# Performance work log

Measured on AMD Instinct MI355X. Metric: run time of the kernel, lower is better.

## Reference

```python
import jax, jax.numpy as jnp
import numpy as np
from jax import lax

B, N, DDESC = 8, 256, 128
COST_KP = 1.0
COST_DESC = 1.0
BLOCK = 128  # row block for L1 cdist


def setup_inputs() -> dict:
    key = jax.random.key(0)
    k1, k2, k3, k4, k5 = jax.random.split(key, 5)
    W, H = 640, 480
    wh = jnp.array([W, H], jnp.float32)
    kp1 = jax.random.uniform(k1, (B, N, 2)) * wh          # pixel coords
    kp2 = jax.random.uniform(k2, (B, N, 2)) * wh
    desc1 = jax.random.normal(k3, (B, N, DDESC))
    desc2 = jax.random.normal(k4, (B, N, DDESC))
    theta = jax.random.uniform(k5, (1,)) * (2.0 * jnp.pi)
    return {
        "theta": theta,
        "my_feature": jnp.concatenate([kp1, desc1], -1),
        "my_tf_feature": jnp.concatenate([kp2, desc2], -1),
        "my_width": W,
        "my_height": H,
    }


def _fundamental_8point(p1, p2):
    """Normalized 8-point algorithm (cv2.FM_8POINT): p2^T F p1 = 0, F[2,2]=1."""
    def norm(p):
        m = p.mean(0)
        d = jnp.sqrt(((p - m) ** 2).sum(1)).mean()
        s = jnp.sqrt(2.0) / d
        T = jnp.array([[1.0, 0.0, 0.0], [0.0, 1.0, 0.0], [0.0, 0.0, 0.0]]) * s \
            + jnp.zeros((3, 3)).at[0, 2].set(-s * m[0]).at[1, 2].set(-s * m[1]).at[2, 2].set(1.0)
        return (p - m) * s, T
    x1, T1 = norm(p1)
    x2, T2 = norm(p2)
    u1, v1 = x1[:, 0], x1[:, 1]
    u2, v2 = x2[:, 0], x2[:, 1]
    A = jnp.stack([u2 * u1, u2 * v1, u2, v2 * u1, v2 * v1, v2, u1, v1, jnp.ones_like(u1)], 1)
    _, _, Vt = jnp.linalg.svd(A, full_matrices=False)      # Vt: [9,9]
    Fm = Vt[-1].reshape(3, 3)
    U, S, Vt2 = jnp.linalg.svd(Fm)
    Fm = (U * S.at[2].set(0.0)) @ Vt2                      # enforce rank 2
    Fm = T2.T @ Fm @ T1
    return Fm / Fm[2, 2]


def _cdist_l1(a, b):
    """torch.cdist(p=1) without materializing [M,M,D]; blocked over rows."""
    M, D = a.shape
    ab = a.reshape(M // BLOCK, BLOCK, D)
    rows = lax.map(lambda blk: jnp.abs(blk[:, None, :] - b[None, :, :]).sum(-1), ab)
    return rows.reshape(M, b.shape[0])


def _cost_matrix(theta, my_feature, my_tf_feature, W, H):
    my_kp = my_feature[..., :2]
    my_tf_kp = my_tf_feature[..., :2]
    my_desc = my_feature[..., 2:]
    my_tf_desc = my_tf_feature[..., 2:]

    c, s = jnp.cos(theta[0]), jnp.sin(theta[0])
    zero = jnp.zeros(())
    one = jnp.ones(())
    Tm = jnp.stack([
        jnp.stack([c, -s, zero, zero]),
        jnp.stack([s, c, zero, zero]),
        jnp.stack([zero, zero, one, zero]),
        jnp.stack([zero, zero, zero, one]),
    ])  # make_transformation_M(theta, 0, 0): z-rotation, no translation

    # homogeneous image-centered coords: [B, 4, N]
    all_kp = jnp.stack([
        my_kp[:, :, 0] - 0.5 * W,
        -my_kp[:, :, 1] + 0.5 * H,
        jnp.zeros_like(my_kp[:, :, 0]),
        jnp.ones_like(my_kp[:, :, 0]),
    ], 1)
    cal = jnp.round(jnp.einsum('ij,bjn->bin', Tm, all_kp))[:, :2, :]  # [B,2,N]
    g = cal.transpose(0, 2, 1)                                        # [B,N,2]
    o = jnp.stack([g[..., 0] + 0.5 * W, -g[..., 1] + 0.5 * H], -1)    # back to pixels

    pts1 = my_tf_kp.astype(jnp.int32).reshape(B * N, 2).astype(jnp.float32)
    pts2 = o.astype(jnp.int32).reshape(B * N, 2).astype(jnp.float32)
    F = _fundamental_8point(pts1, pts2)

    ones = jnp.ones((B * N, 1), jnp.float32)
    p1h = jnp.concatenate([pts1, ones], 1)
    p2h = jnp.concatenate([pts2, ones], 1)
    cost_kp = jnp.abs((p1h @ F.astype(jnp.float32)) @ p2h.T)          # [BN, BN]

    cost_desc = _cdist_l1(my_desc.reshape(B * N, -1), my_tf_desc.reshape(B * N, -1))
    C = COST_KP * cost_kp + COST_DESC * cost_desc
    return C.reshape(B, N, B * N)


def _hungarian_np(cost):
    """scipy.optimize.linear_sum_assignment (JV shortest augmenting path), numpy."""
    cost = np.asarray(cost, dtype=np.float64)
    n = cost.shape[0]
    u = np.zeros(n)
    v = np.zeros(n)
    path = np.full(n, -1, dtype=np.int64)
    col4row = np.full(n, -1, dtype=np.int64)
    row4col = np.full(n, -1, dtype=np.int64)
    for cur_row in range(n):
        shortest = np.full(n, np.inf)
        remaining = np.ones(n, dtype=bool)
        SR = []
        i = cur_row
        min_val = 0.0
        sink = -1
        while sink == -1:
            SR.append(i)
            idx = np.nonzero(remaining)[0]
            r = min_val + cost[i, idx] - u[i] - v[idx]
            better = r < shortest[idx]
            bidx = idx[better]
            shortest[bidx] = r[better]
            path[bidx] = i
            jpos = idx[np.argmin(shortest[idx])]
            min_val = shortest[jpos]
            remaining[jpos] = False
            if row4col[jpos] == -1:
                sink = jpos
            else:
                i = row4col[jpos]
        u[cur_row] += min_val
        for i2 in SR:
            if i2 != cur_row:
                u[i2] += min_val - shortest[col4row[i2]]
        scanned = ~remaining
        v[scanned] -= min_val - shortest[scanned]
        j = sink
        while True:
            i2 = path[j]
            row4col[j] = i2
            col4row[i2], j = j, col4row[i2]
            if i2 == cur_row:
                break
    return col4row


def reference(theta, my_feature, my_tf_feature, my_width, my_height):
    C = _cost_matrix(theta, my_feature, my_tf_feature, float(my_width), float(my_height))
    Cn = np.asarray(jax.device_get(C))
    # diagonal [N,N] blocks: C.split(num_kp, -1) -> c[i] in the torch code
    cols = np.stack([_hungarian_np(Cn[i, :, i * N:(i + 1) * N]) for i in range(B)])
    rows = np.tile(np.arange(N), (B, 1))
    matches = jnp.asarray(np.stack([rows, cols], 1), dtype=jnp.int32)  # [B,2,N]
    return C, matches
```

## Files before the change

kernel.cpp:

```cpp
#include <hip/hip_runtime.h>
#include <hip/hip_bf16.h>
#include <cfloat>
#include <math.h>

#define BB 8
#define NN 256
#define BN 2048
#define DD 128
#define FEAT 130

__global__ __launch_bounds__(256) void prep_kernel(
    const float* __restrict__ theta,
    const float* __restrict__ feat1,
    const float* __restrict__ feat2,
    const int* __restrict__ wp, const int* __restrict__ hp,
    float* __restrict__ pts1, float* __restrict__ pts2) {
  int i = blockIdx.x * 256 + threadIdx.x;
  if (i >= BN) return;
  double W = (double)wp[0], H = (double)hp[0];
  double th = (double)theta[0];
  double c = cos(th), s = sin(th);
  double kx = (double)feat1[(size_t)i * FEAT + 0];
  double ky = (double)feat1[(size_t)i * FEAT + 1];
  double x = kx - 0.5 * W;
  double y = -ky + 0.5 * H;
  double calx = rint(c * x - s * y);
  double caly = rint(s * x + c * y);
  double ox = calx + 0.5 * W;
  double oy = -caly + 0.5 * H;
  pts2[2 * i]     = (float)(int)ox;
  pts2[2 * i + 1] = (float)(int)oy;
  pts1[2 * i]     = (float)(int)feat2[(size_t)i * FEAT + 0];
  pts1[2 * i + 1] = (float)(int)feat2[(size_t)i * FEAT + 1];
}

__device__ inline double wred(double x) {
#pragma unroll
  for (int off = 32; off > 0; off >>= 1) x += __shfl_down(x, off, 64);
  return x;
}

#define JROT(P, Q) {                                                          \
  double app_ = __shfl(Bc[P], P);                                             \
  double aqq_ = __shfl(Bc[Q], Q);                                             \
  double apq_ = __shfl(Bc[P], Q);                                             \
  double c_, s_;                                                              \
  if (fabs(apq_) > 1e-300) {                                                  \
    double tau_ = (aqq_ - app_) / (2.0 * apq_);                               \
    double t_ = (tau_ >= 0.0 ? 1.0 : -1.0) / (fabs(tau_) + sqrt(1.0 + tau_ * tau_)); \
    c_ = 1.0 / sqrt(1.0 + t_ * t_);                                           \
    s_ = t_ * c_;                                                             \
  } else { c_ = 1.0; s_ = 0.0; }                                              \
  const int prt_ = (jln == P) ? Q : ((jln == Q) ? P : jln);                   \
  const bool isP_ = (jln == P), isQ_ = (jln == Q);                            \
  _Pragma("unroll")                                                           \
  for (int ii = 0; ii < 9; ++ii) {                                            \
    double ob_ = __shfl(Bc[ii], prt_);                                        \
    double ov_ = __shfl(Vc[ii], prt_);                                        \
    if (isP_) { Bc[ii] = c_ * Bc[ii] - s_ * ob_; Vc[ii] = c_ * Vc[ii] - s_ * ov_; } \
    if (isQ_) { Bc[ii] = s_ * ob_ + c_ * Bc[ii]; Vc[ii] = s_ * ov_ + c_ * Vc[ii]; } \
  }                                                                           \
  { double rp_ = Bc[P], rq_ = Bc[Q];                                          \
    Bc[P] = c_ * rp_ - s_ * rq_; Bc[Q] = s_ * rp_ + c_ * rq_; } }

#define ROT3(P, Q) {                                                          \
  double apq_ = A3[P][Q];                                                     \
  double c_, s_;                                                              \
  if (fabs(apq_) > 1e-300) {                                                  \
    double tau_ = (A3[Q][Q] - A3[P][P]) / (2.0 * apq_);                       \
    double t_ = (tau_ >= 0.0 ? 1.0 : -1.0) / (fabs(tau_) + sqrt(1.0 + tau_ * tau_)); \
    c_ = 1.0 / sqrt(1.0 + t_ * t_); s_ = t_ * c_;                             \
  } else { c_ = 1.0; s_ = 0.0; }                                              \
  _Pragma("unroll")                                                           \
  for (int ii = 0; ii < 3; ++ii) { double a_ = A3[ii][P], b_ = A3[ii][Q];     \
    A3[ii][P] = c_ * a_ - s_ * b_; A3[ii][Q] = s_ * a_ + c_ * b_; }           \
  _Pragma("unroll")                                                           \
  for (int ii = 0; ii < 3; ++ii) { double a_ = A3[P][ii], b_ = A3[Q][ii];     \
    A3[P][ii] = c_ * a_ - s_ * b_; A3[Q][ii] = s_ * a_ + c_ * b_; }           \
  _Pragma("unroll")                                                           \
  for (int ii = 0; ii < 3; ++ii) { double a_ = V3[ii][P], b_ = V3[ii][Q];     \
    V3[ii][P] = c_ * a_ - s_ * b_; V3[ii][Q] = s_ * a_ + c_ * b_; } }

__global__ __launch_bounds__(256) void fmat_kernel(
    const float* __restrict__ pts1f, const float* __restrict__ pts2f,
    double* __restrict__ Fout) {
  __shared__ double sred[6];
  __shared__ double sATA[45];
  __shared__ double sV[9][16];
  __shared__ double sEv[16];
  const int tid = threadIdx.x;
  const int lane = tid & 63;
  if (tid < 6) sred[tid] = 0.0;
  if (tid < 45) sATA[tid] = 0.0;
  __syncthreads();

  double sx1 = 0, sy1 = 0, sx2 = 0, sy2 = 0;
  for (int p = tid; p < BN; p += 256) {
    sx1 += (double)pts1f[2 * p];     sy1 += (double)pts1f[2 * p + 1];
    sx2 += (double)pts2f[2 * p];     sy2 += (double)pts2f[2 * p + 1];
  }
  sx1 = wred(sx1); sy1 = wred(sy1); sx2 = wred(sx2); sy2 = wred(sy2);
  if (lane == 0) {
    atomicAdd(&sred[0], sx1); atomicAdd(&sred[1], sy1);
    atomicAdd(&sred[2], sx2); atomicAdd(&sred[3], sy2);
  }
  __syncthreads();
  const double m1x = sred[0] * (1.0 / BN), m1y = sred[1] * (1.0 / BN);
  const double m2x = sred[2] * (1.0 / BN), m2y = sred[3] * (1.0 / BN);

  double d1 = 0, d2 = 0;
  for (int p = tid; p < BN; p += 256) {
    double ax = (double)pts1f[2 * p] - m1x, ay = (double)pts1f[2 * p + 1] - m1y;
    double bx = (double)pts2f[2 * p] - m2x, by = (double)pts2f[2 * p + 1] - m2y;
    d1 += sqrt(ax * ax + ay * ay);
    d2 += sqrt(bx * bx + by * by);
  }
  d1 = wred(d1); d2 = wred(d2);
  if (lane == 0) { atomicAdd(&sred[4], d1); atomicAdd(&sred[5], d2); }
  __syncthreads();
  const double s1 = sqrt(2.0) / (sred[4] * (1.0 / BN));
  const double s2 = sqrt(2.0) / (sred[5] * (1.0 / BN));

  double acc45[45];
#pragma unroll
  for (int e = 0; e < 45; ++e) acc45[e] = 0.0;
  for (int p = tid; p < BN; p += 256) {
    double u1 = ((double)pts1f[2 * p]     - m1x) * s1;
    double v1 = ((double)pts1f[2 * p + 1] - m1y) * s1;
    double u2 = ((double)pts2f[2 * p]     - m2x) * s2;
    double v2 = ((double)pts2f[2 * p + 1] - m2y) * s2;
    double r[9] = {u2 * u1, u2 * v1, u2, v2 * u1, v2 * v1, v2, u1, v1, 1.0};
#pragma unroll
    for (int a = 0; a < 9; ++a)
#pragma unroll
      for (int b = a; b < 9; ++b)
        acc45[9 * a - (a * (a - 1)) / 2 + (b - a)] += r[a] * r[b];
  }
#pragma unroll
  for (int e = 0; e < 45; ++e) {
    double vv = wred(acc45[e]);
    if (lane == 0) atomicAdd(&sATA[e], vv);
  }
  __syncthreads();

  if (tid < 64) {
    const int jln = tid;
    double Bc[9], Vc[9];
#pragma unroll
    for (int i2 = 0; i2 < 9; ++i2) {
      if (jln < 9) {
        int a = i2 < jln ? i2 : jln;
        int b = i2 < jln ? jln : i2;
        Bc[i2] = sATA[9 * a - (a * (a - 1)) / 2 + (b - a)];
      } else Bc[i2] = 0.0;
      Vc[i2] = (i2 == jln) ? 1.0 : 0.0;
    }
    for (int sw = 0; sw < 7; ++sw) {
      JROT(0,1) JROT(0,2) JROT(0,3) JROT(0,4) JROT(0,5) JROT(0,6) JROT(0,7) JROT(0,8)
      JROT(1,2) JROT(1,3) JROT(1,4) JROT(1,5) JROT(1,6) JROT(1,7) JROT(1,8)
      JROT(2,3) JROT(2,4) JROT(2,5) JROT(2,6) JROT(2,7) JROT(2,8)
      JROT(3,4) JROT(3,5) JROT(3,6) JROT(3,7) JROT(3,8)
      JROT(4,5) JROT(4,6) JROT(4,7) JROT(4,8)
      JROT(5,6) JROT(5,7) JROT(5,8)
      JROT(6,7) JROT(6,8)
      JROT(7,8)
    }
    double ev = 0.0;
#pragma unroll
    for (int i2 = 0; i2 < 9; ++i2) if (jln == i2) ev = Bc[i2];
    if (jln < 9) {
      sEv[jln] = ev;
#pragma unroll
      for (int i2 = 0; i2 < 9; ++i2) sV[i2][jln] = Vc[i2];
    }
  }
  __syncthreads();

  if (tid == 0) {
    int jm = 0; double be = sEv[0];
#pragma unroll
    for (int jj = 1; jj < 9; ++jj) if (sEv[jj] < be) { be = sEv[jj]; jm = jj; }
    double F0[9];
#pragma unroll
    for (int i2 = 0; i2 < 9; ++i2) F0[i2] = sV[i2][jm];
    double M00 = F0[0], M01 = F0[1], M02 = F0[2];
    double M10 = F0[3], M11 = F0[4], M12 = F0[5];
    double M20 = F0[6], M21 = F0[7], M22 = F0[8];
    double A3[3][3], V3[3][3];
    A3[0][0] = M00*M00 + M10*M10 + M20*M20;
    A3[0][1] = M00*M01 + M10*M11 + M20*M21;
    A3[0][2] = M00*M02 + M10*M12 + M20*M22;
    A3[1][1] = M01*M01 + M11*M11 + M21*M21;
    A3[1][2] = M01*M02 + M11*M12 + M21*M22;
    A3[2][2] = M02*M02 + M12*M12 + M22*M22;
    A3[1][0] = A3[0][1]; A3[2][0] = A3[0][2]; A3[2][1] = A3[1][2];
#pragma unroll
    for (int ii = 0; ii < 3; ++ii)
#pragma unroll
      for (int jj = 0; jj < 3; ++jj) V3[ii][jj] = (ii == jj) ? 1.0 : 0.0;
    for (int sw = 0; sw < 10; ++sw) { ROT3(0,1) ROT3(0,2) ROT3(1,2) }
    double w0 = A3[0][0], w1 = A3[1][1], w2 = A3[2][2];
    double vx, vy, vz;
    if (w0 <= w1 && w0 <= w2)      { vx = V3[0][0]; vy = V3[1][0]; vz = V3[2][0]; }
    else if (w1 <= w2)             { vx = V3[0][1]; vy = V3[1][1]; vz = V3[2][1]; }
    else                           { vx = V3[0][2]; vy = V3[1][2]; vz = V3[2][2]; }
    double Mv0 = M00 * vx + M01 * vy + M02 * vz;
    double Mv1 = M10 * vx + M11 * vy + M12 * vz;
    double Mv2 = M20 * vx + M21 * vy + M22 * vz;
    double F200 = M00 - Mv0 * vx, F201 = M01 - Mv0 * vy, F202 = M02 - Mv0 * vz;
    double F210 = M10 - Mv1 * vx, F211 = M11 - Mv1 * vy, F212 = M12 - Mv1 * vz;
    double F220 = M20 - Mv2 * vx, F221 = M21 - Mv2 * vy, F222 = M22 - Mv2 * vz;
    double R00 = s2 * F200, R01 = s2 * F201, R02 = s2 * F202;
    double R10 = s2 * F210, R11 = s2 * F211, R12 = s2 * F212;
    double R20 = -s2 * m2x * F200 - s2 * m2y * F210 + F220;
    double R21 = -s2 * m2x * F201 - s2 * m2y * F211 + F221;
    double R22 = -s2 * m2x * F202 - s2 * m2y * F212 + F222;
    double D00 = s1 * R00, D10 = s1 * R10, D20 = s1 * R20;
    double D01 = s1 * R01, D11 = s1 * R11, D21 = s1 * R21;
    double D02 = -s1 * m1x * R00 - s1 * m1y * R01 + R02;
    double D12 = -s1 * m1x * R10 - s1 * m1y * R11 + R12;
    double D22 = -s1 * m1x * R20 - s1 * m1y * R21 + R22;
    Fout[0] = D00 / D22; Fout[1] = D01 / D22; Fout[2] = D02 / D22;
    Fout[3] = D10 / D22; Fout[4] = D11 / D22; Fout[5] = D12 / D22;
    Fout[6] = D20 / D22; Fout[7] = D21 / D22; Fout[8] = D22 / D22;
  }
}

__global__ __launch_bounds__(256) void cost_kernel(
    const float* __restrict__ feat1,
    const float* __restrict__ feat2,
    const float* __restrict__ pts1,
    const float* __restrict__ pts2,
    const double* __restrict__ Fd,
    float* __restrict__ Cout) {
  __shared__ float D1[128][68];
  __shared__ float D2[128][68];
  __shared__ float a0s[64], a1s[64], a2s[64], p2xs[64], p2ys[64];
  const int tid = threadIdx.x;
  const int rowbase = blockIdx.y * 64;
  const int colbase = blockIdx.x * 64;
#pragma unroll
  for (int it = 0; it < 32; ++it) {
    int idx = it * 256 + tid;
    int r = idx >> 7, k = idx & 127;
    D1[k][r] = feat1[(size_t)(rowbase + r) * FEAT + 2 + k];
    D2[k][r] = feat2[(size_t)(colbase + r) * FEAT + 2 + k];
  }
  if (tid < 64) {
    float x1 = pts1[2 * (rowbase + tid)], y1 = pts1[2 * (rowbase + tid) + 1];
    a0s[tid] = (float)(Fd[0] * x1 + Fd[3] * y1 + Fd[6]);
    a1s[tid] = (float)(Fd[1] * x1 + Fd[4] * y1 + Fd[7]);
    a2s[tid] = (float)(Fd[2] * x1 + Fd[5] * y1 + Fd[8]);
    p2xs[tid] = pts2[2 * (colbase + tid)];
    p2ys[tid] = pts2[2 * (colbase + tid) + 1];
  }
  __syncthreads();
  const int tx = tid & 15, ty = tid >> 4;
  float acc[4][4] = {};
#pragma unroll 4
  for (int k = 0; k < 128; ++k) {
    float4 av = *(const float4*)&D1[k][ty * 4];
    float4 bv = *(const float4*)&D2[k][tx * 4];
    float ar[4] = {av.x, av.y, av.z, av.w};
    float br[4] = {bv.x, bv.y, bv.z, bv.w};
#pragma unroll
    for (int r = 0; r < 4; ++r)
#pragma unroll
      for (int c = 0; c < 4; ++c)
        acc[r][c] += fabsf(ar[r] - br[c]);
  }
#pragma unroll
  for (int r = 0; r < 4; ++r) {
    int row = rowbase + ty * 4 + r;
    float a0 = a0s[ty * 4 + r], a1 = a1s[ty * 4 + r], a2 = a2s[ty * 4 + r];
    float4 o;
    float* op = &o.x;
#pragma unroll
    for (int c = 0; c < 4; ++c) {
      float kp = fabsf(a0 * p2xs[tx * 4 + c] + a1 * p2ys[tx * 4 + c] + a2);
      op[c] = acc[r][c] + kp;
    }
    *(float4*)&Cout[(size_t)row * BN + colbase + tx * 4] = o;
  }
}

#define NROWS_C 152

__device__ __forceinline__ unsigned long long sortkey(double d) {
  long long b = __double_as_longlong(d);
  long long m = (b >> 63) | (long long)0x8000000000000000LL;
  return (unsigned long long)(b ^ m);
}
__device__ __forceinline__ double unsortkey(unsigned long long k) {
  unsigned long long m = ((long long)k < 0) ? 0x8000000000000000ULL
                                            : 0xFFFFFFFFFFFFFFFFULL;
  return __longlong_as_double((long long)(k ^ m));
}

template<int CTRL, int RM>
__device__ __forceinline__ unsigned dppm32(unsigned x) {
  int y = __builtin_amdgcn_update_dpp((int)x, (int)x, CTRL, RM, 0xF, false);
  unsigned u = (unsigned)y;
  return u < x ? u : x;
}
template<int CTRL, int RM>
__device__ __forceinline__ unsigned long long dppm64(unsigned long long x) {
  int lo = (int)(unsigned)x, hi = (int)(unsigned)(x >> 32);
  int lo2 = __builtin_amdgcn_update_dpp(lo, lo, CTRL, RM, 0xF, false);
  int hi2 = __builtin_amdgcn_update_dpp(hi, hi, CTRL, RM, 0xF, false);
  unsigned long long y =
      ((unsigned long long)(unsigned)hi2 << 32) | (unsigned)lo2;
  return y < x ? y : x;
}

__device__ __forceinline__ unsigned wave_min_u32(unsigned x) {
  unsigned h = dppm32<0x111, 0xF>(x);
  h = dppm32<0x112, 0xF>(h);
  h = dppm32<0x114, 0xF>(h);
  h = dppm32<0x118, 0xF>(h);
  h = dppm32<0x142, 0xA>(h);
  h = dppm32<0x143, 0xC>(h);
  return (unsigned)__builtin_amdgcn_readlane((int)h, 63);
}
__device__ __forceinline__ unsigned long long wave_min_u64(unsigned long long x) {
  unsigned long long h = dppm64<0x111, 0xF>(x);
  h = dppm64<0x112, 0xF>(h);
  h = dppm64<0x114, 0xF>(h);
  h = dppm64<0x118, 0xF>(h);
  h = dppm64<0x142, 0xA>(h);
  h = dppm64<0x143, 0xC>(h);
  unsigned lo = (unsigned)__builtin_amdgcn_readlane((int)(unsigned)h, 63);
  unsigned hi = (unsigned)__builtin_amdgcn_readlane((int)(unsigned)(h >> 32), 63);
  return ((unsigned long long)hi << 32) | lo;
}

__device__ __forceinline__ double rl64(double x, int l) {
  long long bb = __double_as_longlong(x);
  int lo = __builtin_amdgcn_readlane((int)(bb & 0xFFFFFFFFLL), l);
  int hi = __builtin_amdgcn_readlane((int)(bb >> 32), l);
  return __longlong_as_double(((long long)hi << 32) | (unsigned)lo);
}
__device__ __forceinline__ unsigned long long rdpair(unsigned ghi, unsigned glo, int l) {
  return ((unsigned long long)(unsigned)__builtin_amdgcn_readlane((int)ghi, l) << 32)
       | (unsigned)__builtin_amdgcn_readlane((int)glo, l);
}

__device__ __forceinline__ unsigned long long reduce_key(unsigned long long kl) {
  unsigned hi = (unsigned)(kl >> 32);
  unsigned mh = wave_min_u32(hi);
  unsigned long long bal = __ballot(hi == mh);
  if (__builtin_popcountll(bal) == 1)
    return rdpair(hi, (unsigned)kl, (int)__builtin_ctzll(bal));
  return wave_min_u64(kl);
}

struct RPick { unsigned long long g; int wl; int li; };

__device__ __forceinline__ RPick reduce_pick(unsigned long long kl, int myli) {
  unsigned hi = (unsigned)(kl >> 32);
  unsigned mh = wave_min_u32(hi);
  unsigned long long bal = __ballot(hi == mh);
  unsigned long long g; int wl;
  if (__builtin_popcountll(bal) == 1) {
    wl = (int)__builtin_ctzll(bal);
    g = rdpair(hi, (unsigned)kl, wl);
  } else {
    g = wave_min_u64(kl);
    bal = __ballot(kl == g);
    wl = (int)__builtin_ctzll(bal);
  }
  int li = __builtin_amdgcn_readlane(myli, wl);
  RPick r; r.g = g; r.wl = wl; r.li = li; return r;
}

#define UPD(K, CK, KK, PP) {                                           \
  double d_ = (base + (double)(CK)) - v##K;                            \
  unsigned long long nk_ = sortkey(d_);                                \
  bool a_ = ((rem >> (K)) & 1u) && (nk_ < (KK));                       \
  (KK) = a_ ? nk_ : (KK);                                              \
  (PP) = a_ ? i : (PP); }

#define ROWLOAD(I) ((I) < NROWS_C ? *(const float4*)&rcache[(I)][lane * 4]   \
                                  : *(const float4*)(Cb + (size_t)(I) * BN + lane * 4))

#define R4C_OF(LI) ((LI) == 0 ? r4c0 : (LI) == 1 ? r4c1 : (LI) == 2 ? r4c2 : r4c3)
#define U4_OF(LI)  ((LI) == 0 ? u40  : (LI) == 1 ? u41  : (LI) == 2 ? u42  : u43)

__global__ __launch_bounds__(64) void hungarian_kernel(
    const float* __restrict__ C, float* __restrict__ out_matches) {
  const int b = blockIdx.x;
  const int lane = threadIdx.x;
  __shared__ float rcache[NROWS_C][NN];
  __shared__ int c4r_lds[NN];
  __shared__ double u_sd[NN];
  const float* Cb = C + (size_t)b * NN * BN + (size_t)b * NN;

  for (int t = lane; t < NROWS_C * (NN / 4); t += 64) {
    int r = t >> 6, q = t & 63;
    *(float4*)&rcache[r][q * 4] = *(const float4*)(Cb + (size_t)r * BN + q * 4);
  }
  for (int r = lane; r < NN; r += 64) c4r_lds[r] = -1;
  __syncthreads();

  for (int i = 0; i < NN; ++i) {
    float4 cr = ROWLOAD(i);
    float m01 = fminf(cr.x, cr.y), m23 = fminf(cr.z, cr.w);
    unsigned gm = wave_min_u32(__float_as_uint(fminf(m01, m23)));
    if (lane == 0) u_sd[i] = (double)__uint_as_float(gm);
  }
  __syncthreads();

  double v0, v1, v2, v3;
  {
    double c0 = DBL_MAX, c1 = DBL_MAX, c2 = DBL_MAX, c3 = DBL_MAX;
    for (int i = 0; i < NN; ++i) {
      float4 cr = ROWLOAD(i);
      double uu = u_sd[i];
      double s0 = (double)cr.x - uu; c0 = s0 < c0 ? s0 : c0;
      double s1 = (double)cr.y - uu; c1 = s1 < c1 ? s1 : c1;
      double s2 = (double)cr.z - uu; c2 = s2 < c2 ? s2 : c2;
      double s3 = (double)cr.w - uu; c3 = s3 < c3 ? s3 : c3;
    }
    v0 = c0; v1 = c1; v2 = c2; v3 = c3;
  }

  __syncthreads();
  for (int i = 0; i < NN; ++i) {
    float4 cr = ROWLOAD(i);
    double s0 = (double)cr.x - v0, s1 = (double)cr.y - v1;
    double s2 = (double)cr.z - v2, s3 = (double)cr.w - v3;
    double ma = s0 < s1 ? s0 : s1, mb = s2 < s3 ? s2 : s3;
    unsigned long long kl = sortkey(ma < mb ? ma : mb);
    unsigned long long g = reduce_key(kl);
    if (lane == 0) u_sd[i] = unsortkey(g);
  }
  __syncthreads();

  int am0 = 0, am1 = 0, am2 = 0, am3 = 0;
  {
    double c0 = DBL_MAX, c1 = DBL_MAX, c2 = DBL_MAX, c3 = DBL_MAX;
    for (int i = 0; i < NN; ++i) {
      float4 cr = ROWLOAD(i);
      double uu = u_sd[i];
      double s0 = (double)cr.x - uu; if (s0 < c0) { c0 = s0; am0 = i; }
      double s1 = (double)cr.y - uu; if (s1 < c1) { c1 = s1; am1 = i; }
      double s2 = (double)cr.z - uu; if (s2 < c2) { c2 = s2; am2 = i; }
      double s3 = (double)cr.w - uu; if (s3 < c3) { c3 = s3; am3 = i; }
    }
    v0 = c0; v1 = c1; v2 = c2; v3 = c3;
  }

  int r4c0, r4c1, r4c2, r4c3;
  { int old = atomicCAS(&c4r_lds[am0], -1, lane * 4 + 0); r4c0 = (old == -1) ? am0 : -1; }
  { int old = atomicCAS(&c4r_lds[am1], -1, lane * 4 + 1); r4c1 = (old == -1) ? am1 : -1; }
  { int old = atomicCAS(&c4r_lds[am2], -1, lane * 4 + 2); r4c2 = (old == -1) ? am2 : -1; }
  { int old = atomicCAS(&c4r_lds[am3], -1, lane * 4 + 3); r4c3 = (old == -1) ? am3 : -1; }
  __syncthreads();
  int c4r0 = c4r_lds[lane * 4 + 0];
  int c4r1 = c4r_lds[lane * 4 + 1];
  int c4r2 = c4r_lds[lane * 4 + 2];
  int c4r3 = c4r_lds[lane * 4 + 3];
  double u40 = (r4c0 >= 0) ? u_sd[r4c0] : 0.0;
  double u41 = (r4c1 >= 0) ? u_sd[r4c1] : 0.0;
  double u42 = (r4c2 >= 0) ? u_sd[r4c2] : 0.0;
  double u43 = (r4c3 >= 0) ? u_sd[r4c3] : 0.0;

  const unsigned long long KMAX = 0xFFFFFFFFFFFFFFFFULL;

  for (int cur = 0; cur < NN; ++cur) {
    {
      int sl = cur & 3, ow = cur >> 2;
      int myc = (sl == 0) ? c4r0 : (sl == 1) ? c4r1 : (sl == 2) ? c4r2 : c4r3;
      if (__builtin_amdgcn_readlane(myc, ow) >= 0) continue;
    }
    unsigned long long k0 = KMAX, k1 = KMAX, k2 = KMAX, k3 = KMAX;
    int p0 = -1, p1 = -1, p2 = -1, p3 = -1;
    double shp0 = 0, shp1 = 0, shp2 = 0, shp3 = 0;
    unsigned rem = 0xFu;
    double minval = 0.0;
    const double ucur0 = u_sd[cur];
    double ui = ucur0;
    int i = cur;
    int sink = -1;
    while (true) {
      float4 cr = ROWLOAD(i);
      double base = minval - ui;
      UPD(0, cr.x, k0, p0)
      UPD(1, cr.y, k1, p1)
      UPD(2, cr.z, k2, p2)
      UPD(3, cr.w, k3, p3)
      unsigned long long m01 = k0 < k1 ? k0 : k1;
      unsigned long long m23 = k2 < k3 ? k2 : k3;
      unsigned long long kl = m01 < m23 ? m01 : m23;
      int myli = (k0 == kl) ? 0 : (k1 == kl) ? 1 : (k2 == kl) ? 2 : 3;
      RPick rm = reduce_pick(kl, myli);
      minval = unsortkey(rm.g);
      int jpos = rm.wl * 4 + rm.li;
      int mr = R4C_OF(rm.li);
      int rc = __builtin_amdgcn_readlane(mr, rm.wl);
      double mu = U4_OF(rm.li);
      if (lane == rm.wl) {
        if (rm.li == 0)      { k0 = KMAX; shp0 = minval; }
        else if (rm.li == 1) { k1 = KMAX; shp1 = minval; }
        else if (rm.li == 2) { k2 = KMAX; shp2 = minval; }
        else                 { k3 = KMAX; shp3 = minval; }
        rem &= ~(1u << rm.li);
      }
      if (rc < 0) { sink = jpos; break; }
      ui = rl64(mu, rm.wl);
      i = rc;
    }
    if (!(rem & 1u)) { double dl = minval - shp0; v0 -= dl; if (r4c0 >= 0) u40 += dl; }
    if (!(rem & 2u)) { double dl = minval - shp1; v1 -= dl; if (r4c1 >= 0) u41 += dl; }
    if (!(rem & 4u)) { double dl = minval - shp2; v2 -= dl; if (r4c2 >= 0) u42 += dl; }
    if (!(rem & 8u)) { double dl = minval - shp3; v3 -= dl; if (r4c3 >= 0) u43 += dl; }
    int j = sink;
    while (true) {
      int slot = j & 3, ow = j >> 2;
      int myp = (slot == 0) ? p0 : (slot == 1) ? p1 : (slot == 2) ? p2 : p3;
      int i2 = __builtin_amdgcn_readlane(myp, ow);
      int s2 = i2 & 3, ow2 = i2 >> 2;
      int myc = (s2 == 0) ? c4r0 : (s2 == 1) ? c4r1 : (s2 == 2) ? c4r2 : c4r3;
      int jn = __builtin_amdgcn_readlane(myc, ow2);
      double newu;
      if (i2 == cur) {
        newu = ucur0 + minval;
      } else {
        int slj = jn & 3, owj = jn >> 2;
        double myuj = (slj == 0) ? u40 : (slj == 1) ? u41
                    : (slj == 2) ? u42 : u43;
        newu = rl64(myuj, owj);
      }
      if (lane == ow) {
        if (slot == 0) { r4c0 = i2; u40 = newu; }
        else if (slot == 1) { r4c1 = i2; u41 = newu; }
        else if (slot == 2) { r4c2 = i2; u42 = newu; }
        else { r4c3 = i2; u43 = newu; }
      }
      if (lane == ow2) {
        if (s2 == 0) c4r0 = j; else if (s2 == 1) c4r1 = j;
        else if (s2 == 2) c4r2 = j; else c4r3 = j;
      }
      if (i2 == cur) break;
      j = jn;
    }
  }

  float4 ridx, cidx;
  ridx.x = (float)(lane * 4 + 0); ridx.y = (float)(lane * 4 + 1);
  ridx.z = (float)(lane * 4 + 2); ridx.w = (float)(lane * 4 + 3);
  cidx.x = (float)c4r0; cidx.y = (float)c4r1;
  cidx.z = (float)c4r2; cidx.w = (float)c4r3;
  *(float4*)&out_matches[b * 2 * NN + lane * 4] = ridx;
  *(float4*)&out_matches[b * 2 * NN + NN + lane * 4] = cidx;
}

extern "C" void kernel_launch(void* const* d_in, const int* in_sizes, int n_in,
                              void* d_out, int out_size, void* d_ws, size_t ws_size,
                              hipStream_t stream) {
  const float* theta = (const float*)d_in[0];
  const float* feat1 = (const float*)d_in[1];
  const float* feat2 = (const float*)d_in[2];
  const int* wp = (const int*)d_in[3];
  const int* hp = (const int*)d_in[4];
  float* out = (float*)d_out;

  float* pts1 = (float*)d_ws;
  float* pts2 = pts1 + 2 * BN;
  double* Fd = (double*)(pts2 + 2 * BN);

  prep_kernel<<<BN / 256, 256, 0, stream>>>(theta, feat1, feat2, wp, hp, pts1, pts2);
  fmat_kernel<<<1, 256, 0, stream>>>(pts1, pts2, Fd);
  dim3 grid(BN / 64, BN / 64);
  cost_kernel<<<grid, 256, 0, stream>>>(feat1, feat2, pts1, pts2, Fd, out);
  hungarian_kernel<<<BB, 64, 0, stream>>>(out, out + (size_t)BN * BN);
}
```

Before: 2.013 ms.

## Prefetch next Dijkstra row early, build free-row list, drop row-reduction init passes

The shortest-augmenting-path inner loop now issues the load of the next row as soon as the chosen column's assigned row is known, before the sortkey reconstruction and bookkeeping, so LDS or global latency overlaps with other work. The outer loop walks a compacted list of free rows built with a ballot instead of testing every row and skipping assigned ones. Two of the four initialization passes over the cost matrix (the column-min pass and the row re-reduction pass) are removed. Dropping that re-reduction changes the initial duals and the greedy assignment, which may leave more free rows for the augmentation phase.

```diff
diff --git a/kernel.cpp b/kernel.cpp
--- a/kernel.cpp
+++ b/kernel.cpp
@@ -345,34 +345,6 @@
        | (unsigned)__builtin_amdgcn_readlane((int)glo, l);
 }
 
-__device__ __forceinline__ unsigned long long reduce_key(unsigned long long kl) {
-  unsigned hi = (unsigned)(kl >> 32);
-  unsigned mh = wave_min_u32(hi);
-  unsigned long long bal = __ballot(hi == mh);
-  if (__builtin_popcountll(bal) == 1)
-    return rdpair(hi, (unsigned)kl, (int)__builtin_ctzll(bal));
-  return wave_min_u64(kl);
-}
-
-struct RPick { unsigned long long g; int wl; int li; };
-
-__device__ __forceinline__ RPick reduce_pick(unsigned long long kl, int myli) {
-  unsigned hi = (unsigned)(kl >> 32);
-  unsigned mh = wave_min_u32(hi);
-  unsigned long long bal = __ballot(hi == mh);
-  unsigned long long g; int wl;
-  if (__builtin_popcountll(bal) == 1) {
-    wl = (int)__builtin_ctzll(bal);
-    g = rdpair(hi, (unsigned)kl, wl);
-  } else {
-    g = wave_min_u64(kl);
-    bal = __ballot(kl == g);
-    wl = (int)__builtin_ctzll(bal);
-  }
-  int li = __builtin_amdgcn_readlane(myli, wl);
-  RPick r; r.g = g; r.wl = wl; r.li = li; return r;
-}
-
 #define UPD(K, CK, KK, PP) {                                           \
   double d_ = (base + (double)(CK)) - v##K;                            \
   unsigned long long nk_ = sortkey(d_);                                \
@@ -393,6 +365,7 @@
   __shared__ float rcache[NROWS_C][NN];
   __shared__ int c4r_lds[NN];
   __shared__ double u_sd[NN];
+  __shared__ int flist[NN];
   const float* Cb = C + (size_t)b * NN * BN + (size_t)b * NN;
 
   for (int t = lane; t < NROWS_C * (NN / 4); t += 64) {
@@ -411,31 +384,6 @@
   __syncthreads();
 
   double v0, v1, v2, v3;
-  {
-    double c0 = DBL_MAX, c1 = DBL_MAX, c2 = DBL_MAX, c3 = DBL_MAX;
-    for (int i = 0; i < NN; ++i) {
-      float4 cr = ROWLOAD(i);
-      double uu = u_sd[i];
-      double s0 = (double)cr.x - uu; c0 = s0 < c0 ? s0 : c0;
-      double s1 = (double)cr.y - uu; c1 = s1 < c1 ? s1 : c1;
-      double s2 = (double)cr.z - uu; c2 = s2 < c2 ? s2 : c2;
-      double s3 = (double)cr.w - uu; c3 = s3 < c3 ? s3 : c3;
-    }
-    v0 = c0; v1 = c1; v2 = c2; v3 = c3;
-  }
-
-  __syncthreads();
-  for (int i = 0; i < NN; ++i) {
-    float4 cr = ROWLOAD(i);
-    double s0 = (double)cr.x - v0, s1 = (double)cr.y - v1;
-    double s2 = (double)cr.z - v2, s3 = (double)cr.w - v3;
-    double ma = s0 < s1 ? s0 : s1, mb = s2 < s3 ? s2 : s3;
-    unsigned long long kl = sortkey(ma < mb ? ma : mb);
-    unsigned long long g = reduce_key(kl);
-    if (lane == 0) u_sd[i] = unsortkey(g);
-  }
-  __syncthreads();
-
   int am0 = 0, am1 = 0, am2 = 0, am3 = 0;
   {
     double c0 = DBL_MAX, c1 = DBL_MAX, c2 = DBL_MAX, c3 = DBL_MAX;
@@ -465,14 +413,20 @@
   double u42 = (r4c2 >= 0) ? u_sd[r4c2] : 0.0;
   double u43 = (r4c3 >= 0) ? u_sd[r4c3] : 0.0;
 
+  int totfree = 0;
+  for (int r0 = 0; r0 < NN; r0 += 64) {
+    bool fr = (c4r_lds[r0 + lane] < 0);
+    unsigned long long mask = __ballot(fr);
+    int idx = totfree + __builtin_popcountll(mask & ((1ULL << lane) - 1ULL));
+    if (fr) flist[idx] = r0 + lane;
+    totfree += (int)__builtin_popcountll(mask);
+  }
+  __syncthreads();
+
   const unsigned long long KMAX = 0xFFFFFFFFFFFFFFFFULL;
 
-  for (int cur = 0; cur < NN; ++cur) {
-    {
-      int sl = cur & 3, ow = cur >> 2;
-      int myc = (sl == 0) ? c4r0 : (sl == 1) ? c4r1 : (sl == 2) ? c4r2 : c4r3;
-      if (__builtin_amdgcn_readlane(myc, ow) >= 0) continue;
-    }
+  for (int fi = 0; fi < totfree; ++fi) {
+    const int cur = flist[fi];
     unsigned long long k0 = KMAX, k1 = KMAX, k2 = KMAX, k3 = KMAX;
     int p0 = -1, p1 = -1, p2 = -1, p3 = -1;
     double shp0 = 0, shp1 = 0, shp2 = 0, shp3 = 0;
@@ -482,8 +436,8 @@
     double ui = ucur0;
     int i = cur;
     int sink = -1;
+    float4 cr = ROWLOAD(cur);
     while (true) {
-      float4 cr = ROWLOAD(i);
       double base = minval - ui;
       UPD(0, cr.x, k0, p0)
       UPD(1, cr.y, k1, p1)
@@ -493,22 +447,38 @@
       unsigned long long m23 = k2 < k3 ? k2 : k3;
       unsigned long long kl = m01 < m23 ? m01 : m23;
       int myli = (k0 == kl) ? 0 : (k1 == kl) ? 1 : (k2 == kl) ? 2 : 3;
-      RPick rm = reduce_pick(kl, myli);
-      minval = unsortkey(rm.g);
-      int jpos = rm.wl * 4 + rm.li;
-      int mr = R4C_OF(rm.li);
-      int rc = __builtin_amdgcn_readlane(mr, rm.wl);
-      double mu = U4_OF(rm.li);
-      if (lane == rm.wl) {
-        if (rm.li == 0)      { k0 = KMAX; shp0 = minval; }
-        else if (rm.li == 1) { k1 = KMAX; shp1 = minval; }
-        else if (rm.li == 2) { k2 = KMAX; shp2 = minval; }
-        else                 { k3 = KMAX; shp3 = minval; }
-        rem &= ~(1u << rm.li);
+      unsigned hi = (unsigned)(kl >> 32);
+      unsigned mh = wave_min_u32(hi);
+      unsigned long long bal = __ballot(hi == mh);
+      int wl; unsigned long long g; bool fast;
+      if (__builtin_popcountll(bal) == 1) {
+        wl = (int)__builtin_ctzll(bal);
+        fast = true; g = 0;
+      } else {
+        g = wave_min_u64(kl);
+        bal = __ballot(kl == g);
+        wl = (int)__builtin_ctzll(bal);
+        fast = false;
       }
-      if (rc < 0) { sink = jpos; break; }
-      ui = rl64(mu, rm.wl);
+      int li = __builtin_amdgcn_readlane(myli, wl);
+      int myrc = R4C_OF(li);
+      int rc = __builtin_amdgcn_readlane(myrc, wl);
+      float4 nxt;
+      if (rc >= 0) nxt = ROWLOAD(rc);
+      if (fast) g = rdpair(hi, (unsigned)kl, wl);
+      minval = unsortkey(g);
+      double mu = U4_OF(li);
+      if (lane == wl) {
+        if (li == 0)      { k0 = KMAX; shp0 = minval; }
+        else if (li == 1) { k1 = KMAX; shp1 = minval; }
+        else if (li == 2) { k2 = KMAX; shp2 = minval; }
+        else              { k3 = KMAX; shp3 = minval; }
+        rem &= ~(1u << li);
+      }
+      if (rc < 0) { sink = wl * 4 + li; break; }
+      ui = rl64(mu, wl);
       i = rc;
+      cr = nxt;
     }
     if (!(rem & 1u)) { double dl = minval - shp0; v0 -= dl; if (r4c0 >= 0) u40 += dl; }
     if (!(rem & 2u)) { double dl = minval - shp1; v1 -= dl; if (r4c1 >= 0) u41 += dl; }
```

New measurement: 1.985 ms. Within noise of the previous version (-1.4%).
